# Optimization experiments

Measured on AMD Instinct MI355X. Metric: run time of the kernel, lower is better.

The kernel has to match this reference:

```python
import jax, jax.numpy as jnp
import numpy as np

EPS = 1e-08


def setup_inputs() -> dict:
    key = jax.random.key(0)
    X = jax.random.normal(key, (16384, 768), dtype=jnp.float32)
    return {"X": X}


def reference(X) -> jnp.ndarray:
    # L2-normalize rows (torch F.normalize with eps: divide by max(norm, eps))
    norms = jnp.linalg.norm(X, axis=-1, keepdims=True)
    Xn = X / jnp.maximum(norms, EPS)

    n = Xn.shape[0]
    # pairwise inner products [n, n]; mask self-similarity on diagonal with -1
    dots = Xn @ Xn.T
    dots = jnp.where(jnp.eye(n, dtype=bool), jnp.float32(-1.0), dots)
    I = jnp.argmax(dots, axis=1)  # nearest neighbor index per row

    # torch PairwiseDistance(2, eps): ||x - y + eps||_2
    diff = Xn - Xn[I] + EPS
    distances = jnp.linalg.norm(diff, axis=-1)

    # loss_type == 'standard'
    loss = -jnp.mean(jnp.log(distances + EPS))
    return loss
```

## Files before the change

kernel.cpp:

```cpp
#include <hip/hip_runtime.h>
#include <hip/hip_bf16.h>
#include <stdint.h>
#include <math.h>

#define NR 16384
#define DIM 768
#define KEPS 1e-8f

#define BM 128
#define BK 64
#define NB (NR / BM)
#define KT (DIM / BK)
#define NTILES (NB * (NB + 1) / 2)

typedef __attribute__((ext_vector_type(4))) float f32x4;
typedef _Float16 f16x8 __attribute__((ext_vector_type(8)));

__device__ inline uint32_t fkey(float f) {
    union { float f; uint32_t u; } v; v.f = f;
    return (v.u & 0x80000000u) ? ~v.u : (v.u | 0x80000000u);
}
__device__ inline float unkey(uint32_t k) {
    union { uint32_t u; float f; } v;
    v.u = (k & 0x80000000u) ? (k ^ 0x80000000u) : ~k;
    return v.f;
}

__device__ inline void gload16(const ushort* g, const ushort* l) {
    __builtin_amdgcn_global_load_lds(
        (const __attribute__((address_space(1))) void*)g,
        (__attribute__((address_space(3))) void*)l,
        16, 0, 0);
}

__global__ __launch_bounds__(256) void k_norm(const float* __restrict__ X,
                                              ushort* __restrict__ Xn) {
    const int wid = threadIdx.x >> 6, lane = threadIdx.x & 63;
    const int row = blockIdx.x * 4 + wid;
    const float4* xr = (const float4*)(X + (size_t)row * DIM) + lane * 3;
    float4 a = xr[0], b = xr[1], c = xr[2];
    float s = a.x*a.x + a.y*a.y + a.z*a.z + a.w*a.w
            + b.x*b.x + b.y*b.y + b.z*b.z + b.w*b.w
            + c.x*c.x + c.y*c.y + c.z*c.z + c.w*c.w;
#pragma unroll
    for (int m = 32; m >= 1; m >>= 1) s += __shfl_xor(s, m);
    const float rn = 1.0f / fmaxf(sqrtf(s), KEPS);
    float v[12] = {a.x,a.y,a.z,a.w,b.x,b.y,b.z,b.w,c.x,c.y,c.z,c.w};
    uint32_t p[6];
#pragma unroll
    for (int i = 0; i < 6; ++i) {
        union { _Float16 h[2]; uint32_t u; } pk;
        pk.h[0] = (_Float16)(v[2*i] * rn);
        pk.h[1] = (_Float16)(v[2*i+1] * rn);
        p[i] = pk.u;
    }
    uint2* dst = (uint2*)(Xn + (size_t)row * DIM + lane * 12);
    dst[0] = make_uint2(p[0], p[1]);
    dst[1] = make_uint2(p[2], p[3]);
    dst[2] = make_uint2(p[4], p[5]);
}

__global__ __launch_bounds__(256) void k_init(uint32_t* __restrict__ nnkey) {
    nnkey[blockIdx.x * 256 + threadIdx.x] = fkey(-2.0f);
}

__global__ __launch_bounds__(256, 4) void k_maxdot(const ushort* __restrict__ Xn,
                                                   uint32_t* __restrict__ nnkey) {
    __shared__ ushort lA[BM * BK];
    __shared__ ushort lB[BM * BK];
    const int tid  = threadIdx.x;
    const int lane = tid & 63, wid = tid >> 6;
    const int wr = wid >> 1, wc = wid & 1;
    const int l15 = lane & 15, lhi = lane >> 4;

    int t = (int)blockIdx.x;
    t = (t & 7) * (NTILES / 8) + (t >> 3);
    float disc = 66049.0f - 8.0f * (float)t;
    int rb = (int)((257.0f - sqrtf(disc)) * 0.5f);
    if (rb > NB - 1) rb = NB - 1;
    if (rb < 0) rb = 0;
    while (rb > 0 && rb * (257 - rb) / 2 > t) --rb;
    while ((rb + 1) * (257 - (rb + 1)) / 2 <= t) ++rb;
    const int cb = rb + (t - rb * (257 - rb) / 2);
    const int rowbase = rb * BM;
    const int colbase = cb * BM;
    const bool diag = (rb == cb);

    const int s_row  = tid >> 3;
    const int s_slot = tid & 7;

    f32x4 acc[4][4];
    const f32x4 z = {0.f, 0.f, 0.f, 0.f};
#pragma unroll
    for (int i = 0; i < 4; ++i)
#pragma unroll
        for (int j = 0; j < 4; ++j) acc[i][j] = z;

    for (int kt = 0; kt < KT; ++kt) {
#pragma unroll
        for (int it = 0; it < 4; ++it) {
            const int r = it * 32 + s_row;
            const size_t koff = (size_t)kt * BK + (size_t)((s_slot ^ (r & 7)) << 3);
            gload16(Xn + (size_t)(rowbase + r) * DIM + koff, &lA[it * 2048 + wid * 512]);
            gload16(Xn + (size_t)(colbase + r) * DIM + koff, &lB[it * 2048 + wid * 512]);
        }
        __syncthreads();
#pragma unroll
        for (int ks = 0; ks < 2; ++ks) {
            f16x8 af[4], bg[4];
#pragma unroll
            for (int mf = 0; mf < 4; ++mf) {
                const int r = wr * 64 + mf * 16 + l15;
                const int slot = (ks * 4 + lhi) ^ (r & 7);
                af[mf] = *(const f16x8*)(lA + r * BK + slot * 8);
            }
#pragma unroll
            for (int nf = 0; nf < 4; ++nf) {
                const int r = wc * 64 + nf * 16 + l15;
                const int slot = (ks * 4 + lhi) ^ (r & 7);
                bg[nf] = *(const f16x8*)(lB + r * BK + slot * 8);
            }
#pragma unroll
            for (int mf = 0; mf < 4; ++mf)
#pragma unroll
                for (int nf = 0; nf < 4; ++nf)
                    acc[mf][nf] = __builtin_amdgcn_mfma_f32_16x16x32_f16(
                        af[mf], bg[nf], acc[mf][nf], 0, 0, 0);
        }
        __syncthreads();
    }

    if (diag) {
#pragma unroll
        for (int mf = 0; mf < 4; ++mf)
#pragma unroll
            for (int nf = 0; nf < 4; ++nf)
#pragma unroll
                for (int rr = 0; rr < 4; ++rr) {
                    const int rl = wr * 64 + mf * 16 + lhi * 4 + rr;
                    const int cl = wc * 64 + nf * 16 + l15;
                    if (rl == cl) acc[mf][nf][rr] = -1.0f;
                }
    }

#pragma unroll
    for (int mf = 0; mf < 4; ++mf) {
#pragma unroll
        for (int rr = 0; rr < 4; ++rr) {
            float v = fmaxf(fmaxf(acc[mf][0][rr], acc[mf][1][rr]),
                            fmaxf(acc[mf][2][rr], acc[mf][3][rr]));
            v = fmaxf(v, __shfl_xor(v, 1));
            v = fmaxf(v, __shfl_xor(v, 2));
            v = fmaxf(v, __shfl_xor(v, 4));
            v = fmaxf(v, __shfl_xor(v, 8));
            if (l15 == 0) {
                const int r = rowbase + wr * 64 + mf * 16 + lhi * 4 + rr;
                atomicMax(&nnkey[r], fkey(v));
            }
        }
    }

#pragma unroll
    for (int nf = 0; nf < 4; ++nf) {
        float v = -2.0f;
#pragma unroll
        for (int mf = 0; mf < 4; ++mf)
#pragma unroll
            for (int rr = 0; rr < 4; ++rr) v = fmaxf(v, acc[mf][nf][rr]);
        v = fmaxf(v, __shfl_xor(v, 16));
        v = fmaxf(v, __shfl_xor(v, 32));
        if (lhi == 0) {
            const int c = colbase + wc * 64 + nf * 16 + l15;
            atomicMax(&nnkey[c], fkey(v));
        }
    }
}

__global__ __launch_bounds__(256) void k_loss(const uint32_t* __restrict__ nnkey,
                                              float* __restrict__ out) {
    float local = 0.0f;
    for (int r = threadIdx.x; r < NR; r += 256) {
        const float m = unkey(nnkey[r]);
        const float d = sqrtf(fmaxf(2.0f - 2.0f * m, 0.0f));
        local += logf(d + KEPS);
    }
#pragma unroll
    for (int m = 32; m >= 1; m >>= 1) local += __shfl_xor(local, m);
    __shared__ float red[4];
    const int lane = threadIdx.x & 63, wid = threadIdx.x >> 6;
    if (lane == 0) red[wid] = local;
    __syncthreads();
    if (threadIdx.x == 0)
        out[0] = -(red[0] + red[1] + red[2] + red[3]) / (float)NR;
}

extern "C" void kernel_launch(void* const* d_in, const int* in_sizes, int n_in,
                              void* d_out, int out_size, void* d_ws, size_t ws_size,
                              hipStream_t stream) {
    const float* X = (const float*)d_in[0];
    float* out = (float*)d_out;
    ushort* Xn = (ushort*)d_ws;
    uint32_t* nnkey = (uint32_t*)((char*)d_ws + (size_t)NR * DIM * 2);

    k_norm<<<NR / 4, 256, 0, stream>>>(X, Xn);
    k_init<<<NR / 256, 256, 0, stream>>>(nnkey);
    k_maxdot<<<NTILES, 256, 0, stream>>>(Xn, nnkey);
    k_loss<<<1, 256, 0, stream>>>(nnkey, out);
}
```

Before: 315.1 us.

## Use 256x256 tiles with 1024-thread blocks and double-buffered LDS staging

The output tile grows from 128x128 to 256x256 and each block now runs 16 waves, which cuts the number of triangular tiles and the redundant global loads of Xn. The K loop now double-buffers shared memory: the next K-slice is issued with global_load_lds before computing the current one, synchronised with vmcnt waits and raw barriers. The LDS layout becomes two 32-wide halves with a new XOR swizzle. The risks are lower occupancy, since 64KB of LDS and 1024 threads per block allow few resident blocks, and a fragile manual waitcnt scheme.

```diff
diff --git a/kernel.cpp b/kernel.cpp
--- a/kernel.cpp
+++ b/kernel.cpp
@@ -7,10 +7,10 @@
 #define DIM 768
 #define KEPS 1e-8f
 
-#define BM 128
-#define BK 64
-#define NB (NR / BM)
-#define KT (DIM / BK)
+#define BMT 256
+#define BKT 64
+#define NB (NR / BMT)
+#define KT (DIM / BKT)
 #define NTILES (NB * (NB + 1) / 2)
 
 typedef __attribute__((ext_vector_type(4))) float f32x4;
@@ -64,30 +64,25 @@
     nnkey[blockIdx.x * 256 + threadIdx.x] = fkey(-2.0f);
 }
 
-__global__ __launch_bounds__(256, 4) void k_maxdot(const ushort* __restrict__ Xn,
-                                                   uint32_t* __restrict__ nnkey) {
-    __shared__ ushort lA[BM * BK];
-    __shared__ ushort lB[BM * BK];
+__global__ __launch_bounds__(1024, 4) void k_maxdot(const ushort* __restrict__ Xn,
+                                                    uint32_t* __restrict__ nnkey) {
+    __shared__ ushort sA[2][2][256 * 32];
+    __shared__ ushort sB[2][2][256 * 32];
     const int tid  = threadIdx.x;
     const int lane = tid & 63, wid = tid >> 6;
-    const int wr = wid >> 1, wc = wid & 1;
-    const int l15 = lane & 15, lhi = lane >> 4;
+    const int l15 = lane & 15, lhi = (lane >> 4) & 3;
+    const int wr = wid >> 2, wc = wid & 3;
 
     int t = (int)blockIdx.x;
     t = (t & 7) * (NTILES / 8) + (t >> 3);
-    float disc = 66049.0f - 8.0f * (float)t;
-    int rb = (int)((257.0f - sqrtf(disc)) * 0.5f);
+    int rb = (int)((129.0f - sqrtf(16641.0f - 8.0f * (float)t)) * 0.5f);
+    if (rb < 0) rb = 0;
     if (rb > NB - 1) rb = NB - 1;
-    if (rb < 0) rb = 0;
-    while (rb > 0 && rb * (257 - rb) / 2 > t) --rb;
-    while ((rb + 1) * (257 - (rb + 1)) / 2 <= t) ++rb;
-    const int cb = rb + (t - rb * (257 - rb) / 2);
-    const int rowbase = rb * BM;
-    const int colbase = cb * BM;
-    const bool diag = (rb == cb);
-
-    const int s_row  = tid >> 3;
-    const int s_slot = tid & 7;
+    while (rb > 0 && rb * (129 - rb) / 2 > t) --rb;
+    while ((rb + 1) * (129 - (rb + 1)) / 2 <= t) ++rb;
+    const int cb = rb + (t - rb * (129 - rb) / 2);
+    const int rowbase = rb * BMT;
+    const int colbase = cb * BMT;
 
     f32x4 acc[4][4];
     const f32x4 z = {0.f, 0.f, 0.f, 0.f};
@@ -96,30 +91,30 @@
 #pragma unroll
         for (int j = 0; j < 4; ++j) acc[i][j] = z;
 
-    for (int kt = 0; kt < KT; ++kt) {
-#pragma unroll
-        for (int it = 0; it < 4; ++it) {
-            const int r = it * 32 + s_row;
-            const size_t koff = (size_t)kt * BK + (size_t)((s_slot ^ (r & 7)) << 3);
-            gload16(Xn + (size_t)(rowbase + r) * DIM + koff, &lA[it * 2048 + wid * 512]);
-            gload16(Xn + (size_t)(colbase + r) * DIM + koff, &lB[it * 2048 + wid * 512]);
-        }
-        __syncthreads();
+    const int sR = tid >> 2;
+    const int sC = (tid & 3) ^ ((sR >> 1) & 3);
+    auto STAGE = [&](int buf, int kt) {
+        const size_t kbase = (size_t)kt * BKT;
+        const ushort* gA0 = Xn + (size_t)(rowbase + sR) * DIM + kbase + sC * 8;
+        const ushort* gA1 = gA0 + 32;
+        const ushort* gB0 = Xn + (size_t)(colbase + sR) * DIM + kbase + sC * 8;
+        const ushort* gB1 = gB0 + 32;
+        gload16(gA0, &sA[buf][0][wid * 512]);
+        gload16(gA1, &sA[buf][1][wid * 512]);
+        gload16(gB0, &sB[buf][0][wid * 512]);
+        gload16(gB1, &sB[buf][1][wid * 512]);
+    };
+    auto RD = [&](const ushort* region, int r) -> f16x8 {
+        return *(const f16x8*)(region + r * 32 + ((lhi ^ ((r >> 1) & 3)) << 3));
+    };
+    auto COMPUTE = [&](int b) {
 #pragma unroll
         for (int ks = 0; ks < 2; ++ks) {
             f16x8 af[4], bg[4];
 #pragma unroll
-            for (int mf = 0; mf < 4; ++mf) {
-                const int r = wr * 64 + mf * 16 + l15;
-                const int slot = (ks * 4 + lhi) ^ (r & 7);
-                af[mf] = *(const f16x8*)(lA + r * BK + slot * 8);
-            }
-#pragma unroll
-            for (int nf = 0; nf < 4; ++nf) {
-                const int r = wc * 64 + nf * 16 + l15;
-                const int slot = (ks * 4 + lhi) ^ (r & 7);
-                bg[nf] = *(const f16x8*)(lB + r * BK + slot * 8);
-            }
+            for (int mf = 0; mf < 4; ++mf) af[mf] = RD(sA[b][ks], wr * 64 + mf * 16 + l15);
+#pragma unroll
+            for (int nf = 0; nf < 4; ++nf) bg[nf] = RD(sB[b][ks], wc * 64 + nf * 16 + l15);
 #pragma unroll
             for (int mf = 0; mf < 4; ++mf)
 #pragma unroll
@@ -127,10 +122,24 @@
                     acc[mf][nf] = __builtin_amdgcn_mfma_f32_16x16x32_f16(
                         af[mf], bg[nf], acc[mf][nf], 0, 0, 0);
         }
-        __syncthreads();
-    }
-
-    if (diag) {
+    };
+
+    STAGE(0, 0);
+    for (int kt = 0; kt < KT - 1; ++kt) {
+        STAGE((kt + 1) & 1, kt + 1);
+        asm volatile("s_waitcnt vmcnt(4)" ::: "memory");
+        __builtin_amdgcn_s_barrier();
+        __builtin_amdgcn_sched_barrier(0);
+        COMPUTE(kt & 1);
+        __builtin_amdgcn_s_barrier();
+        __builtin_amdgcn_sched_barrier(0);
+    }
+    asm volatile("s_waitcnt vmcnt(0)" ::: "memory");
+    __builtin_amdgcn_s_barrier();
+    __builtin_amdgcn_sched_barrier(0);
+    COMPUTE((KT - 1) & 1);
+
+    if (rb == cb) {
 #pragma unroll
         for (int mf = 0; mf < 4; ++mf)
 #pragma unroll
@@ -144,7 +153,7 @@
     }
 
 #pragma unroll
-    for (int mf = 0; mf < 4; ++mf) {
+    for (int mf = 0; mf < 4; ++mf)
 #pragma unroll
         for (int rr = 0; rr < 4; ++rr) {
             float v = fmaxf(fmaxf(acc[mf][0][rr], acc[mf][1][rr]),
@@ -158,7 +167,6 @@
                 atomicMax(&nnkey[r], fkey(v));
             }
         }
-    }
 
 #pragma unroll
     for (int nf = 0; nf < 4; ++nf) {
@@ -169,7 +177,7 @@
             for (int rr = 0; rr < 4; ++rr) v = fmaxf(v, acc[mf][nf][rr]);
         v = fmaxf(v, __shfl_xor(v, 16));
         v = fmaxf(v, __shfl_xor(v, 32));
-        if (lhi == 0) {
+        if ((lane >> 4) == 0) {
             const int c = colbase + wc * 64 + nf * 16 + l15;
             atomicMax(&nnkey[c], fkey(v));
         }
@@ -204,6 +212,6 @@
 
     k_norm<<<NR / 4, 256, 0, stream>>>(X, Xn);
     k_init<<<NR / 256, 256, 0, stream>>>(nnkey);
-    k_maxdot<<<NTILES, 256, 0, stream>>>(Xn, nnkey);
+    k_maxdot<<<NTILES, 1024, 0, stream>>>(Xn, nnkey);
     k_loss<<<1, 256, 0, stream>>>(nnkey, out);
 }
```

Measured after the change: 332.7 us. 1.06x slower.

## Use FP8 MFMA for similarity search and refine nearest-neighbor distance in fp32

Applied to the files above, without the earlier changes.

Normalized rows are now quantized to FP8 (e4m3) in software, and the pairwise max-dot GEMM runs on fp8 MFMA with 8-bit LDS tiles, halving operand bytes and raising matrix throughput. Because fp8 dot values are too coarse to give the distance directly, the atomic max now packs the argmax column index with the value in a 64-bit key. A new refine kernel recomputes each row's exact fp32 distance to that neighbor from the original input. The cost is an extra kernel, 64-bit atomics, argmax tracking in the epilogue, and a risk that fp8 rounding picks a different neighbor than the exact reference.

```diff
diff --git a/kernel.cpp b/kernel.cpp
--- a/kernel.cpp
+++ b/kernel.cpp
@@ -14,27 +14,43 @@
 #define NTILES (NB * (NB + 1) / 2)
 
 typedef __attribute__((ext_vector_type(4))) float f32x4;
-typedef _Float16 f16x8 __attribute__((ext_vector_type(8)));
 
 __device__ inline uint32_t fkey(float f) {
     union { float f; uint32_t u; } v; v.f = f;
     return (v.u & 0x80000000u) ? ~v.u : (v.u | 0x80000000u);
 }
-__device__ inline float unkey(uint32_t k) {
-    union { uint32_t u; float f; } v;
-    v.u = (k & 0x80000000u) ? (k ^ 0x80000000u) : ~k;
-    return v.f;
-}
-
-__device__ inline void gload16(const ushort* g, const ushort* l) {
+
+__device__ inline unsigned long long pack_vc(float v, int c) {
+    return ((unsigned long long)fkey(v) << 32) | (unsigned)c;
+}
+
+__device__ inline void gload16(const uint8_t* g, const uint8_t* l) {
     __builtin_amdgcn_global_load_lds(
         (const __attribute__((address_space(1))) void*)g,
         (__attribute__((address_space(3))) void*)l,
         16, 0, 0);
 }
 
+__device__ inline uint8_t f2fp8(float f) {
+    union { float f; uint32_t u; } v; v.f = f;
+    const uint8_t s = (uint8_t)((v.u >> 24) & 0x80u);
+    float a = fabsf(f);
+    if (a >= 448.0f) return s | 0x7E;
+    if (a < 0.015625f) {
+        int q = (int)rintf(a * 512.0f);
+        if (q >= 8) return s | 0x08;
+        return s | (uint8_t)q;
+    }
+    int ex; float m = frexpf(a, &ex);
+    int E = ex + 6;
+    int frac = (int)rintf(m * 16.0f - 8.0f);
+    if (frac >= 8) { frac = 0; ++E; if (E > 15) return s | 0x7E; }
+    return s | (uint8_t)(E << 3) | (uint8_t)frac;
+}
+
 __global__ __launch_bounds__(256) void k_norm(const float* __restrict__ X,
-                                              ushort* __restrict__ Xn) {
+                                              uint8_t* __restrict__ Xn,
+                                              float* __restrict__ norms) {
     const int wid = threadIdx.x >> 6, lane = threadIdx.x & 63;
     const int row = blockIdx.x * 4 + wid;
     const float4* xr = (const float4*)(X + (size_t)row * DIM) + lane * 3;
@@ -44,30 +60,27 @@
             + c.x*c.x + c.y*c.y + c.z*c.z + c.w*c.w;
 #pragma unroll
     for (int m = 32; m >= 1; m >>= 1) s += __shfl_xor(s, m);
-    const float rn = 1.0f / fmaxf(sqrtf(s), KEPS);
+    const float n = sqrtf(s);
+    if (lane == 0) norms[row] = n;
+    const float rn = 1.0f / fmaxf(n, KEPS);
     float v[12] = {a.x,a.y,a.z,a.w,b.x,b.y,b.z,b.w,c.x,c.y,c.z,c.w};
-    uint32_t p[6];
-#pragma unroll
-    for (int i = 0; i < 6; ++i) {
-        union { _Float16 h[2]; uint32_t u; } pk;
-        pk.h[0] = (_Float16)(v[2*i] * rn);
-        pk.h[1] = (_Float16)(v[2*i+1] * rn);
-        p[i] = pk.u;
-    }
-    uint2* dst = (uint2*)(Xn + (size_t)row * DIM + lane * 12);
-    dst[0] = make_uint2(p[0], p[1]);
-    dst[1] = make_uint2(p[2], p[3]);
-    dst[2] = make_uint2(p[4], p[5]);
-}
-
-__global__ __launch_bounds__(256) void k_init(uint32_t* __restrict__ nnkey) {
-    nnkey[blockIdx.x * 256 + threadIdx.x] = fkey(-2.0f);
-}
-
-__global__ __launch_bounds__(256, 4) void k_maxdot(const ushort* __restrict__ Xn,
-                                                   uint32_t* __restrict__ nnkey) {
-    __shared__ ushort lA[BM * BK];
-    __shared__ ushort lB[BM * BK];
+    uint8_t q[12];
+#pragma unroll
+    for (int i = 0; i < 12; ++i) q[i] = f2fp8(v[i] * rn);
+    uint32_t* dst = (uint32_t*)(Xn + (size_t)row * DIM + lane * 12);
+    dst[0] = (uint32_t)q[0] | ((uint32_t)q[1] << 8) | ((uint32_t)q[2] << 16) | ((uint32_t)q[3] << 24);
+    dst[1] = (uint32_t)q[4] | ((uint32_t)q[5] << 8) | ((uint32_t)q[6] << 16) | ((uint32_t)q[7] << 24);
+    dst[2] = (uint32_t)q[8] | ((uint32_t)q[9] << 8) | ((uint32_t)q[10] << 16) | ((uint32_t)q[11] << 24);
+}
+
+__global__ __launch_bounds__(256) void k_init(unsigned long long* __restrict__ nn64) {
+    nn64[blockIdx.x * 256 + threadIdx.x] = pack_vc(-2.0f, 0);
+}
+
+__global__ __launch_bounds__(256, 4) void k_maxdot(const uint8_t* __restrict__ Xn,
+                                                   unsigned long long* __restrict__ nn64) {
+    __shared__ uint8_t lA[BM * BK];
+    __shared__ uint8_t lB[BM * BK];
     const int tid  = threadIdx.x;
     const int lane = tid & 63, wid = tid >> 6;
     const int wr = wid >> 1, wc = wid & 1;
@@ -86,9 +99,6 @@
     const int colbase = cb * BM;
     const bool diag = (rb == cb);
 
-    const int s_row  = tid >> 3;
-    const int s_slot = tid & 7;
-
     f32x4 acc[4][4];
     const f32x4 z = {0.f, 0.f, 0.f, 0.f};
 #pragma unroll
@@ -96,35 +106,39 @@
 #pragma unroll
         for (int j = 0; j < 4; ++j) acc[i][j] = z;
 
+    const int s_r0 = tid >> 2;
+    const int s_c  = tid & 3;
+
     for (int kt = 0; kt < KT; ++kt) {
 #pragma unroll
-        for (int it = 0; it < 4; ++it) {
-            const int r = it * 32 + s_row;
-            const size_t koff = (size_t)kt * BK + (size_t)((s_slot ^ (r & 7)) << 3);
-            gload16(Xn + (size_t)(rowbase + r) * DIM + koff, &lA[it * 2048 + wid * 512]);
-            gload16(Xn + (size_t)(colbase + r) * DIM + koff, &lB[it * 2048 + wid * 512]);
+        for (int it = 0; it < 2; ++it) {
+            const int r = it * 64 + s_r0;
+            const int c = s_c ^ ((r >> 1) & 3);
+            const size_t koff = (size_t)kt * BK + c * 16;
+            gload16(Xn + (size_t)(rowbase + r) * DIM + koff, lA + it * 4096 + wid * 1024);
+            gload16(Xn + (size_t)(colbase + r) * DIM + koff, lB + it * 4096 + wid * 1024);
         }
         __syncthreads();
 #pragma unroll
         for (int ks = 0; ks < 2; ++ks) {
-            f16x8 af[4], bg[4];
+            long af[4], bg[4];
+            const int s16 = ks * 2 + (lhi >> 1);
+            const int lo8 = (lhi & 1) * 8;
 #pragma unroll
             for (int mf = 0; mf < 4; ++mf) {
                 const int r = wr * 64 + mf * 16 + l15;
-                const int slot = (ks * 4 + lhi) ^ (r & 7);
-                af[mf] = *(const f16x8*)(lA + r * BK + slot * 8);
+                af[mf] = *(const long*)(lA + r * 64 + ((s16 ^ ((r >> 1) & 3)) << 4) + lo8);
             }
 #pragma unroll
             for (int nf = 0; nf < 4; ++nf) {
                 const int r = wc * 64 + nf * 16 + l15;
-                const int slot = (ks * 4 + lhi) ^ (r & 7);
-                bg[nf] = *(const f16x8*)(lB + r * BK + slot * 8);
+                bg[nf] = *(const long*)(lB + r * 64 + ((s16 ^ ((r >> 1) & 3)) << 4) + lo8);
             }
 #pragma unroll
             for (int mf = 0; mf < 4; ++mf)
 #pragma unroll
                 for (int nf = 0; nf < 4; ++nf)
-                    acc[mf][nf] = __builtin_amdgcn_mfma_f32_16x16x32_f16(
+                    acc[mf][nf] = __builtin_amdgcn_mfma_f32_16x16x32_fp8_fp8(
                         af[mf], bg[nf], acc[mf][nf], 0, 0, 0);
         }
         __syncthreads();
@@ -144,46 +158,85 @@
     }
 
 #pragma unroll
-    for (int mf = 0; mf < 4; ++mf) {
+    for (int mf = 0; mf < 4; ++mf)
 #pragma unroll
         for (int rr = 0; rr < 4; ++rr) {
-            float v = fmaxf(fmaxf(acc[mf][0][rr], acc[mf][1][rr]),
-                            fmaxf(acc[mf][2][rr], acc[mf][3][rr]));
-            v = fmaxf(v, __shfl_xor(v, 1));
-            v = fmaxf(v, __shfl_xor(v, 2));
-            v = fmaxf(v, __shfl_xor(v, 4));
-            v = fmaxf(v, __shfl_xor(v, 8));
+            float v = acc[mf][0][rr];
+            int   c = colbase + wc * 64 + l15;
+#pragma unroll
+            for (int nf = 1; nf < 4; ++nf) {
+                const float w2 = acc[mf][nf][rr];
+                const int   c2 = colbase + wc * 64 + nf * 16 + l15;
+                if (w2 > v) { v = w2; c = c2; }
+            }
+#pragma unroll
+            for (int m = 1; m <= 8; m <<= 1) {
+                const float ov = __shfl_xor(v, m);
+                const int   oc = __shfl_xor(c, m);
+                if (ov > v) { v = ov; c = oc; }
+            }
             if (l15 == 0) {
                 const int r = rowbase + wr * 64 + mf * 16 + lhi * 4 + rr;
-                atomicMax(&nnkey[r], fkey(v));
-            }
-        }
-    }
+                atomicMax(&nn64[r], pack_vc(v, c));
+            }
+        }
 
 #pragma unroll
     for (int nf = 0; nf < 4; ++nf) {
-        float v = -2.0f;
+        float v = acc[0][nf][0];
+        int   c = rowbase + wr * 64 + lhi * 4;
 #pragma unroll
         for (int mf = 0; mf < 4; ++mf)
 #pragma unroll
-            for (int rr = 0; rr < 4; ++rr) v = fmaxf(v, acc[mf][nf][rr]);
-        v = fmaxf(v, __shfl_xor(v, 16));
-        v = fmaxf(v, __shfl_xor(v, 32));
-        if (lhi == 0) {
-            const int c = colbase + wc * 64 + nf * 16 + l15;
-            atomicMax(&nnkey[c], fkey(v));
-        }
-    }
-}
-
-__global__ __launch_bounds__(256) void k_loss(const uint32_t* __restrict__ nnkey,
+            for (int rr = 0; rr < 4; ++rr) {
+                if (mf == 0 && rr == 0) continue;
+                const float w2 = acc[mf][nf][rr];
+                const int   c2 = rowbase + wr * 64 + mf * 16 + lhi * 4 + rr;
+                if (w2 > v) { v = w2; c = c2; }
+            }
+#pragma unroll
+        for (int m = 16; m <= 32; m <<= 1) {
+            const float ov = __shfl_xor(v, m);
+            const int   oc = __shfl_xor(c, m);
+            if (ov > v) { v = ov; c = oc; }
+        }
+        if ((lane >> 4) == 0) {
+            const int cc = colbase + wc * 64 + nf * 16 + l15;
+            atomicMax(&nn64[cc], pack_vc(v, c));
+        }
+    }
+}
+
+__global__ __launch_bounds__(256) void k_refine(const float* __restrict__ X,
+                                                const float* __restrict__ norms,
+                                                const unsigned long long* __restrict__ nn64,
+                                                float* __restrict__ logd) {
+    const int wid = threadIdx.x >> 6, lane = threadIdx.x & 63;
+    const int r = blockIdx.x * 4 + wid;
+    const int j = (int)(nn64[r] & 0xFFFFu);
+    const float rnr = 1.0f / fmaxf(norms[r], KEPS);
+    const float rnj = 1.0f / fmaxf(norms[j], KEPS);
+    const float4* xr = (const float4*)(X + (size_t)r * DIM) + lane * 3;
+    const float4* xj = (const float4*)(X + (size_t)j * DIM) + lane * 3;
+    float s = 0.0f;
+#pragma unroll
+    for (int i = 0; i < 3; ++i) {
+        const float4 a = xr[i], b = xj[i];
+        float d;
+        d = a.x * rnr - b.x * rnj + KEPS; s = fmaf(d, d, s);
+        d = a.y * rnr - b.y * rnj + KEPS; s = fmaf(d, d, s);
+        d = a.z * rnr - b.z * rnj + KEPS; s = fmaf(d, d, s);
+        d = a.w * rnr - b.w * rnj + KEPS; s = fmaf(d, d, s);
+    }
+#pragma unroll
+    for (int m = 32; m >= 1; m >>= 1) s += __shfl_xor(s, m);
+    if (lane == 0) logd[r] = logf(sqrtf(s) + KEPS);
+}
+
+__global__ __launch_bounds__(256) void k_loss(const float* __restrict__ logd,
                                               float* __restrict__ out) {
     float local = 0.0f;
-    for (int r = threadIdx.x; r < NR; r += 256) {
-        const float m = unkey(nnkey[r]);
-        const float d = sqrtf(fmaxf(2.0f - 2.0f * m, 0.0f));
-        local += logf(d + KEPS);
-    }
+    for (int r = threadIdx.x; r < NR; r += 256) local += logd[r];
 #pragma unroll
     for (int m = 32; m >= 1; m >>= 1) local += __shfl_xor(local, m);
     __shared__ float red[4];
@@ -199,11 +252,15 @@
                               hipStream_t stream) {
     const float* X = (const float*)d_in[0];
     float* out = (float*)d_out;
-    ushort* Xn = (ushort*)d_ws;
-    uint32_t* nnkey = (uint32_t*)((char*)d_ws + (size_t)NR * DIM * 2);
-
-    k_norm<<<NR / 4, 256, 0, stream>>>(X, Xn);
-    k_init<<<NR / 256, 256, 0, stream>>>(nnkey);
-    k_maxdot<<<NTILES, 256, 0, stream>>>(Xn, nnkey);
-    k_loss<<<1, 256, 0, stream>>>(nnkey, out);
-}
+    uint8_t* Xn = (uint8_t*)d_ws;
+    char* p = (char*)d_ws + (size_t)NR * DIM;
+    float* norms = (float*)p;                 p += (size_t)NR * 4;
+    unsigned long long* nn64 = (unsigned long long*)p; p += (size_t)NR * 8;
+    float* logd = (float*)p;
+
+    k_norm<<<NR / 4, 256, 0, stream>>>(X, Xn, norms);
+    k_init<<<NR / 256, 256, 0, stream>>>(nn64);
+    k_maxdot<<<NTILES, 256, 0, stream>>>(Xn, nn64);
+    k_refine<<<NR / 4, 256, 0, stream>>>(X, norms, nn64, logd);
+    k_loss<<<1, 256, 0, stream>>>(logd, out);
+}
```

Result: slower. 350.6 us (+11.3%).
